# Optimization experiments

Hardware: AMD Instinct MI355X
Metric: run time of the kernel (lower is better)

## Reference

```python
import jax, jax.numpy as jnp
import numpy as np

HEADS = 8
DIM = 512
DIM_HEAD = 64          # dim // 8
LANDMARKS = 256        # dim // 2
PINV_ITERS = 6
KERNEL = 33            # residual depthwise conv kernel
EPS_LN = 1e-5


def setup_inputs() -> dict:
    key = jax.random.key(0)
    ks = jax.random.split(key, 4)
    b, n = 4, 4096
    x = jax.random.normal(ks[0], (b, n, DIM), dtype=jnp.float32)
    ln_g = jnp.ones((DIM,), jnp.float32)
    ln_b = jnp.zeros((DIM,), jnp.float32)
    w_qkv = jax.random.normal(ks[1], (3 * HEADS * DIM_HEAD, DIM), jnp.float32) * 0.02
    w_out = jax.random.normal(ks[2], (DIM, HEADS * DIM_HEAD), jnp.float32) * 0.02
    b_out = jnp.zeros((DIM,), jnp.float32)
    res_w = jax.random.normal(ks[3], (HEADS, 1, KERNEL, 1), jnp.float32) * 0.05
    return {"x": x, "ln_g": ln_g, "ln_b": ln_b, "w_qkv": w_qkv,
            "w_out": w_out, "b_out": b_out, "res_w": res_w}


def _moore_penrose_pinv(x, iters):
    # x: [b, h, m, m]; global (whole-tensor) max of row/col abs-sums, as in torch impl
    abs_x = jnp.abs(x)
    col = abs_x.sum(-1).max()
    row = abs_x.sum(-2).max()
    z = jnp.swapaxes(x, -1, -2) / (col * row)
    I = jnp.eye(x.shape[-1], dtype=x.dtype)
    for _ in range(iters):
        xz = x @ z
        z = 0.25 * z @ (13.0 * I - (xz @ (15.0 * I - (xz @ (7.0 * I - xz)))))
    return z


def reference(x, ln_g, ln_b, w_qkv, w_out, b_out, res_w):
    b, n, d = x.shape
    # pre-norm LayerNorm
    mu = x.mean(-1, keepdims=True)
    var = ((x - mu) ** 2).mean(-1, keepdims=True)
    xn = (x - mu) * jax.lax.rsqrt(var + EPS_LN) * ln_g + ln_b

    qkv = xn @ w_qkv.T                                  # [b, n, 3*h*dh]
    q, k, v = jnp.split(qkv, 3, axis=-1)
    to_heads = lambda t: t.reshape(b, n, HEADS, DIM_HEAD).transpose(0, 2, 1, 3)
    q = to_heads(q) * (DIM_HEAD ** -0.5)                # [b, h, n, dh]
    k = to_heads(k)
    v = to_heads(v)

    m = LANDMARKS
    l = n // m                                          # n chosen multiple of m (no pad)
    q_l = q.reshape(b, HEADS, m, l, DIM_HEAD).mean(3)   # [b, h, m, dh]
    k_l = k.reshape(b, HEADS, m, l, DIM_HEAD).mean(3)

    attn1 = jax.nn.softmax(jnp.einsum('bhid,bhjd->bhij', q, k_l), -1)    # [b,h,n,m]
    attn2 = jax.nn.softmax(jnp.einsum('bhid,bhjd->bhij', q_l, k_l), -1)  # [b,h,m,m]
    attn3 = jax.nn.softmax(jnp.einsum('bhid,bhjd->bhij', q_l, k), -1)    # [b,h,m,n]

    attn2_inv = _moore_penrose_pinv(attn2, PINV_ITERS)
    out = (attn1 @ attn2_inv) @ (attn3 @ v)             # [b, h, n, dh]

    # residual depthwise conv over sequence dim: v as NCHW (C=heads, H=n, W=dh)
    pad = KERNEL // 2
    res = jax.lax.conv_general_dilated(
        v, res_w, window_strides=(1, 1), padding=((pad, pad), (0, 0)),
        dimension_numbers=('NCHW', 'OIHW', 'NCHW'), feature_group_count=HEADS)
    out = out + res

    out = out.transpose(0, 2, 1, 3).reshape(b, n, HEADS * DIM_HEAD)
    out = out @ w_out.T + b_out                         # to_out Linear (dropout=eval identity)
    return x + out
```

## Files before the change

kernel.cpp:

```cpp
#include <hip/hip_runtime.h>
#include <hip/hip_bf16.h>
#include <math.h>


using bf16x8 = __attribute__((ext_vector_type(8))) short;
using f32x4  = __attribute__((ext_vector_type(4))) float;

static __device__ __forceinline__ f32x4 MFMA16(bf16x8 a, bf16x8 b, f32x4 c) {
    return __builtin_amdgcn_mfma_f32_16x16x32_bf16(a, b, c, 0, 0, 0);
}
static __device__ __forceinline__ unsigned short f2b(float f) {
    union { float f; unsigned u; } x; x.f = f;
    unsigned r = x.u + 0x7FFFu + ((x.u >> 16) & 1u);
    return (unsigned short)(r >> 16);
}
static __device__ __forceinline__ float b2f(unsigned short b) {
    union { unsigned u; float f; } x; x.u = ((unsigned)b) << 16; return x.f;
}

__global__ __launch_bounds__(256) void ln_kernel(const float* __restrict__ x,
                                                 const float* __restrict__ g,
                                                 const float* __restrict__ b,
                                                 unsigned short* __restrict__ xn) {
    int row = blockIdx.x;
    const float* xr = x + (size_t)row * 512;
    int t = threadIdx.x;
    float v0 = xr[t], v1 = xr[t + 256];
    __shared__ float red[4];
    float s = v0 + v1;
#pragma unroll
    for (int off = 32; off; off >>= 1) s += __shfl_down(s, off);
    if ((t & 63) == 0) red[t >> 6] = s;
    __syncthreads();
    float mean = (red[0] + red[1] + red[2] + red[3]) * (1.0f / 512.0f);
    __syncthreads();
    float d0 = v0 - mean, d1 = v1 - mean;
    float q2 = d0 * d0 + d1 * d1;
#pragma unroll
    for (int off = 32; off; off >>= 1) q2 += __shfl_down(q2, off);
    if ((t & 63) == 0) red[t >> 6] = q2;
    __syncthreads();
    float var = (red[0] + red[1] + red[2] + red[3]) * (1.0f / 512.0f);
    float inv = rsqrtf(var + 1e-5f);
    unsigned short* o = xn + (size_t)row * 512;
    o[t]       = f2b(d0 * inv * g[t]       + b[t]);
    o[t + 256] = f2b(d1 * inv * g[t + 256] + b[t + 256]);
}

__global__ void cvt_kernel(const float* __restrict__ wqkv, const float* __restrict__ wout,
                           unsigned short* __restrict__ wqkvb, unsigned short* __restrict__ woutb) {
    int idx = blockIdx.x * 256 + threadIdx.x;
    if (idx < 786432) wqkvb[idx] = f2b(wqkv[idx]);
    else woutb[idx - 786432] = f2b(wout[idx - 786432]);
}

template<int MODE>
__global__ __launch_bounds__(256) void gemm_mfma(const unsigned short* __restrict__ A,
                                                 const unsigned short* __restrict__ Bw,
                                                 unsigned short* __restrict__ qb,
                                                 unsigned short* __restrict__ kb,
                                                 unsigned short* __restrict__ vb,
                                                 const float* __restrict__ bias,
                                                 const float* __restrict__ xres,
                                                 float* __restrict__ out) {
    const int K = 512;
    __shared__ unsigned short As[128][40];
    __shared__ unsigned short Bs[128][40];
    int t = threadIdx.x;
    int w = t >> 6, l = t & 63, lr = l & 15, g = l >> 4;
    int wm = w >> 1, wn = w & 1;
    int row0 = blockIdx.x * 128, col0 = blockIdx.y * 128;
    f32x4 acc[4][4];
#pragma unroll
    for (int i = 0; i < 4; ++i)
#pragma unroll
        for (int j = 0; j < 4; ++j) acc[i][j] = (f32x4)0.f;
    int srow = t >> 1, sh = t & 1;
    for (int kt = 0; kt < K; kt += 32) {
        const unsigned short* as = A + (size_t)(row0 + srow) * K + kt + sh * 16;
        *(uint4*)&As[srow][sh * 16]     = *(const uint4*)as;
        *(uint4*)&As[srow][sh * 16 + 8] = *(const uint4*)(as + 8);
        const unsigned short* bs = Bw + (size_t)(col0 + srow) * K + kt + sh * 16;
        *(uint4*)&Bs[srow][sh * 16]     = *(const uint4*)bs;
        *(uint4*)&Bs[srow][sh * 16 + 8] = *(const uint4*)(bs + 8);
        __syncthreads();
        bf16x8 a[4], b[4];
#pragma unroll
        for (int mt = 0; mt < 4; ++mt) a[mt] = *(const bf16x8*)&As[wm * 64 + mt * 16 + lr][g * 8];
#pragma unroll
        for (int nt = 0; nt < 4; ++nt) b[nt] = *(const bf16x8*)&Bs[wn * 64 + nt * 16 + lr][g * 8];
#pragma unroll
        for (int mt = 0; mt < 4; ++mt)
#pragma unroll
            for (int nt = 0; nt < 4; ++nt) acc[mt][nt] = MFMA16(a[mt], b[nt], acc[mt][nt]);
        __syncthreads();
    }
#pragma unroll
    for (int mt = 0; mt < 4; ++mt) {
#pragma unroll
        for (int nt = 0; nt < 4; ++nt) {
#pragma unroll
            for (int r = 0; r < 4; ++r) {
                int row = row0 + wm * 64 + mt * 16 + g * 4 + r;
                int col = col0 + wn * 64 + nt * 16 + lr;
                float val = acc[mt][nt][r];
                if (MODE == 0) {
                    int bb = row >> 12, nn = row & 4095;
                    int which = col >> 9, rem = col & 511;
                    int hh = rem >> 6, dd = rem & 63;
                    size_t di = (((size_t)(bb * 8 + hh)) * 4096 + nn) * 64 + dd;
                    if (which == 0) qb[di] = f2b(val * 0.125f);
                    else if (which == 1) kb[di] = f2b(val);
                    else vb[di] = f2b(val);
                } else {
                    out[(size_t)row * 512 + col] = val + bias[col] + xres[(size_t)row * 512 + col];
                }
            }
        }
    }
}

__global__ __launch_bounds__(256) void vt_kernel(const unsigned short* __restrict__ vb,
                                                 unsigned short* __restrict__ vtb) {
    int n0 = blockIdx.x * 64, bh = blockIdx.y;
    __shared__ unsigned short tl[64][72];
    int t = threadIdx.x;
#pragma unroll
    for (int u = 0; u < 2; ++u) {
        int cid = t * 2 + u;
        int r = cid >> 3, c8 = (cid & 7) << 3;
        uint4 vv = *(const uint4*)(vb + ((size_t)bh * 4096 + n0 + r) * 64 + c8);
        unsigned short* pv = (unsigned short*)&vv;
#pragma unroll
        for (int i = 0; i < 8; ++i) tl[c8 + i][r] = pv[i];
    }
    __syncthreads();
#pragma unroll
    for (int u = 0; u < 2; ++u) {
        int cid = t * 2 + u;
        int r = cid >> 3, c8 = (cid & 7) << 3;
        *(uint4*)(vtb + ((size_t)bh * 64 + r) * 4096 + n0 + c8) = *(uint4*)&tl[r][c8];
    }
}

__global__ void landmark_kernel(const unsigned short* __restrict__ q,
                                const unsigned short* __restrict__ k,
                                float* __restrict__ ql, float* __restrict__ kl,
                                unsigned short* __restrict__ qlb, unsigned short* __restrict__ klb,
                                unsigned short* __restrict__ qll, unsigned short* __restrict__ kll) {
    int idx = blockIdx.x * 256 + threadIdx.x;
    int dh = idx & 63, mi = (idx >> 6) & 255, bh = idx >> 14;
    size_t base = ((size_t)bh * 4096 + mi * 16) * 64 + dh;
    float sq = 0, sk = 0;
#pragma unroll
    for (int j = 0; j < 16; ++j) { sq += b2f(q[base + (size_t)j * 64]); sk += b2f(k[base + (size_t)j * 64]); }
    sq *= 0.0625f; sk *= 0.0625f;
    ql[idx] = sq; kl[idx] = sk;
    unsigned short qh = f2b(sq), kh = f2b(sk);
    qlb[idx] = qh; klb[idx] = kh;
    qll[idx] = f2b(sq - b2f(qh));
    kll[idx] = f2b(sk - b2f(kh));
}

__global__ __launch_bounds__(256) void conv_kernel(const unsigned short* __restrict__ v,
                                                   const float* __restrict__ rw,
                                                   float* __restrict__ outh) {
    int idx = blockIdx.x * 256 + threadIdx.x;
    int o = idx & 7, n = (idx >> 3) & 4095, bh = idx >> 15;
    int h = bh & 7;
    const unsigned short* vb = v + (((size_t)bh) << 18) + o * 8;
    float acc[8];
#pragma unroll
    for (int i = 0; i < 8; ++i) acc[i] = 0.f;
#pragma unroll
    for (int tt = 0; tt < 33; ++tt) {
        int j = n + tt - 16;
        if (j >= 0 && j < 4096) {
            uint4 pv = *(const uint4*)(vb + (size_t)j * 64);
            const unsigned short* pp = (const unsigned short*)&pv;
            float wgt = rw[h * 33 + tt];
#pragma unroll
            for (int i = 0; i < 8; ++i) acc[i] = fmaf(wgt, b2f(pp[i]), acc[i]);
        }
    }
    float4 r0, r1;
    r0.x = acc[0]; r0.y = acc[1]; r0.z = acc[2]; r0.w = acc[3];
    r1.x = acc[4]; r1.y = acc[5]; r1.z = acc[6]; r1.w = acc[7];
    *(float4*)(outh + (size_t)idx * 8)     = r0;
    *(float4*)(outh + (size_t)idx * 8 + 4) = r1;
}

__global__ __launch_bounds__(256) void attn2_mfma(const unsigned short* __restrict__ qlh,
                                                  const unsigned short* __restrict__ qllo,
                                                  const unsigned short* __restrict__ klh,
                                                  const unsigned short* __restrict__ kllo,
                                                  float* __restrict__ a2) {
    int it = blockIdx.x, bh = blockIdx.y;
    __shared__ unsigned short qh_l[64][72], ql_l[64][72];
    __shared__ unsigned short kh_l[128][72], kl_l[128][72];
    int t = threadIdx.x;
    int w = t >> 6, l = t & 63, lr = l & 15, g = l >> 4;
    int i0 = it * 64;
    int srow = t >> 2, sq = t & 3;
    {
        size_t gi = ((size_t)bh * 256 + i0 + srow) * 64 + sq * 16;
        *(uint4*)&qh_l[srow][sq * 16]     = *(const uint4*)(qlh + gi);
        *(uint4*)&qh_l[srow][sq * 16 + 8] = *(const uint4*)(qlh + gi + 8);
        *(uint4*)&ql_l[srow][sq * 16]     = *(const uint4*)(qllo + gi);
        *(uint4*)&ql_l[srow][sq * 16 + 8] = *(const uint4*)(qllo + gi + 8);
    }
    f32x4 p[16];
    float tsum[4] = {0.f, 0.f, 0.f, 0.f};
    bf16x8 ah0, ah1, al0, al1;
#pragma unroll
    for (int ph = 0; ph < 2; ++ph) {
        __syncthreads();
#pragma unroll
        for (int st = 0; st < 2; ++st) {
            int row = st * 64 + srow;
            size_t gi = ((size_t)bh * 256 + ph * 128 + row) * 64 + sq * 16;
            *(uint4*)&kh_l[row][sq * 16]     = *(const uint4*)(klh + gi);
            *(uint4*)&kh_l[row][sq * 16 + 8] = *(const uint4*)(klh + gi + 8);
            *(uint4*)&kl_l[row][sq * 16]     = *(const uint4*)(kllo + gi);
            *(uint4*)&kl_l[row][sq * 16 + 8] = *(const uint4*)(kllo + gi + 8);
        }
        __syncthreads();
        if (ph == 0) {
            ah0 = *(const bf16x8*)&qh_l[w * 16 + lr][g * 8];
            ah1 = *(const bf16x8*)&qh_l[w * 16 + lr][32 + g * 8];
            al0 = *(const bf16x8*)&ql_l[w * 16 + lr][g * 8];
            al1 = *(const bf16x8*)&ql_l[w * 16 + lr][32 + g * 8];
        }
#pragma unroll
        for (int f = 0; f < 8; ++f) {
            bf16x8 bh0 = *(const bf16x8*)&kh_l[f * 16 + lr][g * 8];
            bf16x8 bh1 = *(const bf16x8*)&kh_l[f * 16 + lr][32 + g * 8];
            bf16x8 bl0 = *(const bf16x8*)&kl_l[f * 16 + lr][g * 8];
            bf16x8 bl1 = *(const bf16x8*)&kl_l[f * 16 + lr][32 + g * 8];
            f32x4 s = (f32x4)0.f;
            s = MFMA16(ah0, bh0, s); s = MFMA16(ah1, bh1, s);
            s = MFMA16(ah0, bl0, s); s = MFMA16(ah1, bl1, s);
            s = MFMA16(al0, bh0, s); s = MFMA16(al1, bh1, s);
            f32x4 pe;
#pragma unroll
            for (int r = 0; r < 4; ++r) { pe[r] = __expf(s[r]); tsum[r] += pe[r]; }
            p[ph * 8 + f] = pe;
        }
    }
#pragma unroll
    for (int r = 0; r < 4; ++r) {
#pragma unroll
        for (int m = 1; m < 16; m <<= 1) tsum[r] += __shfl_xor(tsum[r], m);
    }
#pragma unroll
    for (int f = 0; f < 16; ++f) {
#pragma unroll
        for (int r = 0; r < 4; ++r) {
            a2[((size_t)bh * 256 + i0 + w * 16 + g * 4 + r) * 256 + f * 16 + lr] = p[f][r] / tsum[r];
        }
    }
}

__global__ __launch_bounds__(256) void colmax_kernel(const float* __restrict__ a2,
                                                     unsigned* __restrict__ scal) {
    int bh = blockIdx.x, t = threadIdx.x;
    const float* m = a2 + (size_t)bh * 65536;
    float cs = 0;
    for (int i = 0; i < 256; ++i) cs += m[i * 256 + t];
#pragma unroll
    for (int off = 32; off; off >>= 1) cs = fmaxf(cs, __shfl_down(cs, off));
    __shared__ float red[4];
    if ((t & 63) == 0) red[t >> 6] = cs;
    __syncthreads();
    if (t == 0) {
        float mx = fmaxf(fmaxf(red[0], red[1]), fmaxf(red[2], red[3]));
        atomicMax(scal, __float_as_uint(mx));
    }
}

__global__ __launch_bounds__(256) void z0_split(const float* __restrict__ a2,
                                                const float* __restrict__ scal,
                                                float* __restrict__ zf,
                                                unsigned short* __restrict__ zh,
                                                unsigned short* __restrict__ zl) {
    int bh = blockIdx.z;
    int ib = blockIdx.x * 64, jb = blockIdx.y * 64;
    __shared__ float tl[64][65];
    float c = 1.0f / *scal;
    int t = threadIdx.x;
#pragma unroll
    for (int u = 0; u < 16; ++u) {
        int idx = t + 256 * u;
        int r = idx >> 6, cc = idx & 63;
        tl[r][cc] = a2[(size_t)bh * 65536 + (size_t)(jb + r) * 256 + ib + cc];
    }
    __syncthreads();
#pragma unroll
    for (int u = 0; u < 16; ++u) {
        int idx = t + 256 * u;
        int r = idx >> 6, cc = idx & 63;
        float v = tl[cc][r] * c;
        unsigned short hi = f2b(v);
        size_t di = (size_t)bh * 65536 + (size_t)(ib + r) * 256 + jb + cc;
        zf[di] = v;
        zh[di] = hi;
        zl[di] = f2b(v - b2f(hi));
    }
}

__global__ void split_kernel(const float* __restrict__ src,
                             unsigned short* __restrict__ dh,
                             unsigned short* __restrict__ dl) {
    int idx4 = (blockIdx.x * 256 + threadIdx.x) * 4;
    float4 v = *(const float4*)(src + idx4);
    float vv[4] = {v.x, v.y, v.z, v.w};
    ushort4 h4, l4;
    unsigned short* hp = (unsigned short*)&h4;
    unsigned short* lp = (unsigned short*)&l4;
#pragma unroll
    for (int j = 0; j < 4; ++j) {
        unsigned short hi = f2b(vv[j]);
        hp[j] = hi;
        lp[j] = f2b(vv[j] - b2f(hi));
    }
    *(ushort4*)(dh + idx4) = h4;
    *(ushort4*)(dl + idx4) = l4;
}

__global__ __launch_bounds__(256) void bgemm_split2(const unsigned short* __restrict__ Ahg,
                                                    const unsigned short* __restrict__ Alg,
                                                    const unsigned short* __restrict__ Bhg,
                                                    const unsigned short* __restrict__ Blg,
                                                    unsigned short* __restrict__ Dh,
                                                    unsigned short* __restrict__ Dl,
                                                    float* __restrict__ Df,
                                                    const float* __restrict__ Ef,
                                                    float alpha, float gamma) {
    size_t so = (size_t)blockIdx.z * 65536;
    Ahg += so; Alg += so; Bhg += so; Blg += so; Dh += so; Dl += so; Df += so;
    const float* Efp = Ef ? Ef + so : nullptr;
    __shared__ unsigned short Ah[64][40], Al[64][40], Bh2[64][40], Bl2[64][40];
    int t = threadIdx.x;
    int w = t >> 6, l = t & 63, lr = l & 15, g = l >> 4;
    int wm = w >> 1, wn = w & 1;
    int bm = blockIdx.x, bn = blockIdx.y;
    f32x4 acc[2][2];
#pragma unroll
    for (int i = 0; i < 2; ++i)
#pragma unroll
        for (int j = 0; j < 2; ++j) acc[i][j] = (f32x4)0.f;
    int arow = t >> 2, akq = (t & 3) * 8;
    int bkr = t >> 3, bnq = (t & 7) * 8;
    for (int kt = 0; kt < 256; kt += 32) {
        size_t ai = (size_t)(bm * 64 + arow) * 256 + kt + akq;
        *(uint4*)&Ah[arow][akq] = *(const uint4*)(Ahg + ai);
        *(uint4*)&Al[arow][akq] = *(const uint4*)(Alg + ai);
        size_t bi = (size_t)(kt + bkr) * 256 + bn * 64 + bnq;
        uint4 bhv = *(const uint4*)(Bhg + bi);
        uint4 blv = *(const uint4*)(Blg + bi);
        const unsigned short* bhp = (const unsigned short*)&bhv;
        const unsigned short* blp = (const unsigned short*)&blv;
#pragma unroll
        for (int i = 0; i < 8; ++i) {
            Bh2[bnq + i][bkr] = bhp[i];
            Bl2[bnq + i][bkr] = blp[i];
        }
        __syncthreads();
        bf16x8 ah[2], al_[2], bh[2], bl_[2];
#pragma unroll
        for (int mf = 0; mf < 2; ++mf) {
            ah[mf]  = *(const bf16x8*)&Ah[wm * 32 + mf * 16 + lr][g * 8];
            al_[mf] = *(const bf16x8*)&Al[wm * 32 + mf * 16 + lr][g * 8];
        }
#pragma unroll
        for (int nf = 0; nf < 2; ++nf) {
            bh[nf]  = *(const bf16x8*)&Bh2[wn * 32 + nf * 16 + lr][g * 8];
            bl_[nf] = *(const bf16x8*)&Bl2[wn * 32 + nf * 16 + lr][g * 8];
        }
#pragma unroll
        for (int mf = 0; mf < 2; ++mf)
#pragma unroll
            for (int nf = 0; nf < 2; ++nf) {
                acc[mf][nf] = MFMA16(ah[mf], bh[nf], acc[mf][nf]);
                acc[mf][nf] = MFMA16(ah[mf], bl_[nf], acc[mf][nf]);
                acc[mf][nf] = MFMA16(al_[mf], bh[nf], acc[mf][nf]);
            }
        __syncthreads();
    }
#pragma unroll
    for (int mf = 0; mf < 2; ++mf) {
#pragma unroll
        for (int nf = 0; nf < 2; ++nf) {
#pragma unroll
            for (int r = 0; r < 4; ++r) {
                int row = bm * 64 + wm * 32 + mf * 16 + g * 4 + r;
                int col = bn * 64 + wn * 32 + nf * 16 + lr;
                size_t di = (size_t)row * 256 + col;
                float val = alpha * acc[mf][nf][r];
                if (Efp) val = fmaf(gamma, Efp[di], val);
                Df[di] = val;
                unsigned short hi = f2b(val);
                Dh[di] = hi;
                Dl[di] = f2b(val - b2f(hi));
            }
        }
    }
}

__global__ __launch_bounds__(256) void bgemm_w2t(const float* __restrict__ A,
                                                 const float* __restrict__ B,
                                                 unsigned short* __restrict__ w2t) {
    const int M = 256, N = 64, K = 256;
    int s = blockIdx.z;
    int bm = blockIdx.x;
    A += (size_t)s * M * K; B += (size_t)s * K * N;
    __shared__ float As[32][67];
    __shared__ float Bs[32][68];
    int t = threadIdx.x;
    int tm = t & 15, tn = t >> 4;
    float acc[4][4];
#pragma unroll
    for (int i = 0; i < 4; ++i)
#pragma unroll
        for (int j = 0; j < 4; ++j) acc[i][j] = 0.f;
    for (int kt = 0; kt < K; kt += 32) {
#pragma unroll
        for (int u = 0; u < 2; ++u) {
            int fid = t + 256 * u;
            int r = fid >> 3, kg = (fid & 7) << 2;
            float4 av = *(const float4*)(A + (size_t)(bm * 64 + r) * K + kt + kg);
            As[kg + 0][r] = av.x; As[kg + 1][r] = av.y; As[kg + 2][r] = av.z; As[kg + 3][r] = av.w;
            int kr = fid >> 4, cg = (fid & 15) << 2;
            if (cg < N) {
                float4 bv = *(const float4*)(B + (size_t)(kt + kr) * N + cg);
                *(float4*)(&Bs[kr][cg]) = bv;
            }
        }
        __syncthreads();
#pragma unroll
        for (int kk = 0; kk < 32; ++kk) {
            float a[4], bb[4];
#pragma unroll
            for (int i = 0; i < 4; ++i) a[i] = As[kk][tm * 4 + i];
#pragma unroll
            for (int j = 0; j < 4; ++j) bb[j] = Bs[kk][(tn & 15) * 4 + j];
#pragma unroll
            for (int i = 0; i < 4; ++i)
#pragma unroll
                for (int j = 0; j < 4; ++j) acc[i][j] = fmaf(a[i], bb[j], acc[i][j]);
        }
        __syncthreads();
    }
    if (tn < 16) {
#pragma unroll
        for (int i = 0; i < 4; ++i) {
            int r = bm * 64 + tm * 4 + i;
#pragma unroll
            for (int j = 0; j < 4; ++j) {
                int c = tn * 4 + j;
                w2t[(size_t)s * 16384 + (size_t)c * 256 + r] = f2b(acc[i][j]);
            }
        }
    }
}

__global__ __launch_bounds__(256) void attn3v_mfma(const unsigned short* __restrict__ qlb,
                                                   const unsigned short* __restrict__ kb,
                                                   const unsigned short* __restrict__ vtb,
                                                   float* __restrict__ num_part,
                                                   float* __restrict__ den_part) {
    int it = blockIdx.x, js = blockIdx.y, bh = blockIdx.z;
    __shared__ unsigned short k_lds[64][72];
    __shared__ unsigned short v_lds[64][72];
    __shared__ unsigned short p_lds[4][16][72];
    int t = threadIdx.x;
    int w = t >> 6, l = t & 63, lr = l & 15, g = l >> 4;
    int i0 = it * 64;
    const unsigned short* qp = qlb + ((size_t)(bh * 256 + i0 + w * 16 + lr)) * 64 + g * 8;
    bf16x8 aq0 = *(const bf16x8*)qp;
    bf16x8 aq1 = *(const bf16x8*)(qp + 32);
    f32x4 acc[4];
#pragma unroll
    for (int i = 0; i < 4; ++i) acc[i] = (f32x4)0.f;
    float dacc[4] = {0.f, 0.f, 0.f, 0.f};
    int srow = t >> 2, sq = t & 3;
    const size_t kbase = ((size_t)bh * 4096 + js * 1024) * 64;
    const size_t vbase = (size_t)bh * 64 * 4096 + js * 1024;
    for (int st = 0; st < 16; ++st) {
        int j0 = st * 64;
        {
            const unsigned short* src = kb + kbase + (size_t)(j0 + srow) * 64 + sq * 16;
            *(uint4*)&k_lds[srow][sq * 16]     = *(const uint4*)src;
            *(uint4*)&k_lds[srow][sq * 16 + 8] = *(const uint4*)(src + 8);
            const unsigned short* sv = vtb + vbase + (size_t)srow * 4096 + j0 + sq * 16;
            *(uint4*)&v_lds[srow][sq * 16]     = *(const uint4*)sv;
            *(uint4*)&v_lds[srow][sq * 16 + 8] = *(const uint4*)(sv + 8);
        }
        __syncthreads();
        f32x4 sacc[4];
#pragma unroll
        for (int jt = 0; jt < 4; ++jt) {
            bf16x8 bk0 = *(const bf16x8*)&k_lds[jt * 16 + lr][g * 8];
            bf16x8 bk1 = *(const bf16x8*)&k_lds[jt * 16 + lr][32 + g * 8];
            sacc[jt] = MFMA16(aq0, bk0, (f32x4)0.f);
            sacc[jt] = MFMA16(aq1, bk1, sacc[jt]);
        }
        float dr[4] = {0.f, 0.f, 0.f, 0.f};
#pragma unroll
        for (int jt = 0; jt < 4; ++jt) {
#pragma unroll
            for (int r = 0; r < 4; ++r) {
                float p = __expf(sacc[jt][r]);
                p_lds[w][g * 4 + r][jt * 16 + lr] = f2b(p);
                dr[r] += p;
            }
        }
#pragma unroll
        for (int r = 0; r < 4; ++r) {
#pragma unroll
            for (int m = 1; m < 16; m <<= 1) dr[r] += __shfl_xor(dr[r], m);
            dacc[r] += dr[r];
        }
        bf16x8 pa0 = *(const bf16x8*)&p_lds[w][lr][g * 8];
        bf16x8 pa1 = *(const bf16x8*)&p_lds[w][lr][32 + g * 8];
#pragma unroll
        for (int dt = 0; dt < 4; ++dt) {
            bf16x8 bv0 = *(const bf16x8*)&v_lds[dt * 16 + lr][g * 8];
            bf16x8 bv1 = *(const bf16x8*)&v_lds[dt * 16 + lr][32 + g * 8];
            acc[dt] = MFMA16(pa0, bv0, acc[dt]);
            acc[dt] = MFMA16(pa1, bv1, acc[dt]);
        }
        __syncthreads();
    }
    size_t obase = (size_t)(js * 32 + bh) * 256 + i0 + w * 16;
#pragma unroll
    for (int dt = 0; dt < 4; ++dt)
#pragma unroll
        for (int r = 0; r < 4; ++r)
            num_part[(obase + g * 4 + r) * 64 + dt * 16 + lr] = acc[dt][r];
    if (lr == 0) {
#pragma unroll
        for (int r = 0; r < 4; ++r) den_part[obase + g * 4 + r] = dacc[r];
    }
}

__global__ void a3v_combine(const float* __restrict__ num_part,
                            const float* __restrict__ den_part,
                            float* __restrict__ a3v) {
    int idx = blockIdx.x * 256 + threadIdx.x;
    int dh = idx & 63;
    int rest = idx >> 6;
    float n = 0, d = 0;
#pragma unroll
    for (int s = 0; s < 4; ++s) {
        n += num_part[((size_t)s * 8192 + rest) * 64 + dh];
        d += den_part[(size_t)s * 8192 + rest];
    }
    a3v[idx] = n / d;
}

__global__ __launch_bounds__(256) void attn1_mfma(const unsigned short* __restrict__ qb,
                                                  const unsigned short* __restrict__ klb,
                                                  const unsigned short* __restrict__ w2t,
                                                  const float* __restrict__ outh,
                                                  unsigned short* __restrict__ outhb) {
    int it = blockIdx.x, bh = blockIdx.y;
    __shared__ unsigned short k_lds[64][72];
    __shared__ unsigned short v_lds[64][72];
    __shared__ unsigned short p_lds[4][16][72];
    int t = threadIdx.x;
    int w = t >> 6, l = t & 63, lr = l & 15, g = l >> 4;
    int i0 = it * 64;
    const unsigned short* qp = qb + ((size_t)bh * 4096 + i0 + w * 16 + lr) * 64 + g * 8;
    bf16x8 aq0 = *(const bf16x8*)qp;
    bf16x8 aq1 = *(const bf16x8*)(qp + 32);
    f32x4 acc[4];
#pragma unroll
    for (int i = 0; i < 4; ++i) acc[i] = (f32x4)0.f;
    float dacc[4] = {0.f, 0.f, 0.f, 0.f};
    int srow = t >> 2, sq = t & 3;
    for (int st = 0; st < 4; ++st) {
        int j0 = st * 64;
        {
            const unsigned short* src = klb + ((size_t)bh * 256 + j0 + srow) * 64 + sq * 16;
            *(uint4*)&k_lds[srow][sq * 16]     = *(const uint4*)src;
            *(uint4*)&k_lds[srow][sq * 16 + 8] = *(const uint4*)(src + 8);
            const unsigned short* sv = w2t + ((size_t)bh * 64 + srow) * 256 + j0 + sq * 16;
            *(uint4*)&v_lds[srow][sq * 16]     = *(const uint4*)sv;
            *(uint4*)&v_lds[srow][sq * 16 + 8] = *(const uint4*)(sv + 8);
        }
        __syncthreads();
        f32x4 sacc[4];
#pragma unroll
        for (int jt = 0; jt < 4; ++jt) {
            bf16x8 bk0 = *(const bf16x8*)&k_lds[jt * 16 + lr][g * 8];
            bf16x8 bk1 = *(const bf16x8*)&k_lds[jt * 16 + lr][32 + g * 8];
            sacc[jt] = MFMA16(aq0, bk0, (f32x4)0.f);
            sacc[jt] = MFMA16(aq1, bk1, sacc[jt]);
        }
        float dr[4] = {0.f, 0.f, 0.f, 0.f};
#pragma unroll
        for (int jt = 0; jt < 4; ++jt) {
#pragma unroll
            for (int r = 0; r < 4; ++r) {
                float p = __expf(sacc[jt][r]);
                p_lds[w][g * 4 + r][jt * 16 + lr] = f2b(p);
                dr[r] += p;
            }
        }
#pragma unroll
        for (int r = 0; r < 4; ++r) {
#pragma unroll
            for (int m = 1; m < 16; m <<= 1) dr[r] += __shfl_xor(dr[r], m);
            dacc[r] += dr[r];
        }
        bf16x8 pa0 = *(const bf16x8*)&p_lds[w][lr][g * 8];
        bf16x8 pa1 = *(const bf16x8*)&p_lds[w][lr][32 + g * 8];
#pragma unroll
        for (int dt = 0; dt < 4; ++dt) {
            bf16x8 bv0 = *(const bf16x8*)&v_lds[dt * 16 + lr][g * 8];
            bf16x8 bv1 = *(const bf16x8*)&v_lds[dt * 16 + lr][32 + g * 8];
            acc[dt] = MFMA16(pa0, bv0, acc[dt]);
            acc[dt] = MFMA16(pa1, bv1, acc[dt]);
        }
        __syncthreads();
    }
    int bb = bh >> 3, hh = bh & 7;
#pragma unroll
    for (int dt = 0; dt < 4; ++dt) {
#pragma unroll
        for (int r = 0; r < 4; ++r) {
            int row = i0 + w * 16 + g * 4 + r;
            float val = acc[dt][r] / dacc[r]
                      + outh[((size_t)bh * 4096 + row) * 64 + dt * 16 + lr];
            outhb[((size_t)(bb * 4096 + row)) * 512 + hh * 64 + dt * 16 + lr] = f2b(val);
        }
    }
}

extern "C" void kernel_launch(void* const* d_in, const int* in_sizes, int n_in,
                              void* d_out, int out_size, void* d_ws, size_t ws_size,
                              hipStream_t stream) {
    (void)in_sizes; (void)n_in; (void)out_size; (void)ws_size;
    const float* x     = (const float*)d_in[0];
    const float* ln_g  = (const float*)d_in[1];
    const float* ln_b  = (const float*)d_in[2];
    const float* w_qkv = (const float*)d_in[3];
    const float* w_out = (const float*)d_in[4];
    const float* b_out = (const float*)d_in[5];
    const float* res_w = (const float*)d_in[6];
    float* out = (float*)d_out;

    float* ws = (float*)d_ws;
    unsigned short* xnb = (unsigned short*)ws;
    float* num_part = ws;
    float* den_part = ws + 2097152;
    float* a3v      = ws + 2129920;
    unsigned short* outhb = (unsigned short*)ws;
    float* outh = ws + 4194304;
    float* ql   = ws + 12582912;
    float* kl   = ws + 13107200;
    float* a2   = ws + 13631488;
    float* z0f  = ws + 15728640;
    float* z1f  = ws + 17825792;
    float* xzf  = ws + 19922944;
    unsigned* scal = (unsigned*)(ws + 22020096);
    unsigned short* a2h = (unsigned short*)(ws + 22020100);
    unsigned short* a2l = (unsigned short*)(ws + 23068676);
    unsigned short* z0h = (unsigned short*)(ws + 24117252);
    unsigned short* z0l = (unsigned short*)(ws + 25165828);
    unsigned short* z1h = (unsigned short*)(ws + 26214404);
    unsigned short* z1l = (unsigned short*)(ws + 27262980);
    unsigned short* xzh = (unsigned short*)(ws + 28311556);
    unsigned short* xzl = (unsigned short*)(ws + 29360132);
    unsigned short* t1h = (unsigned short*)(ws + 30408708);
    unsigned short* t1l = (unsigned short*)(ws + 31457284);
    unsigned short* t2h = (unsigned short*)(ws + 32505860);
    unsigned short* t2l = (unsigned short*)(ws + 33554436);
    unsigned short* qb  = (unsigned short*)(ws + 34603012);
    unsigned short* kb  = (unsigned short*)(ws + 38797316);
    unsigned short* vb  = (unsigned short*)(ws + 42991620);
    unsigned short* vtb = (unsigned short*)(ws + 47185924);
    unsigned short* qlb   = (unsigned short*)(ws + 51380228);
    unsigned short* klb   = (unsigned short*)(ws + 51642372);
    unsigned short* qll   = (unsigned short*)(ws + 51904516);
    unsigned short* kll   = (unsigned short*)(ws + 52166660);
    unsigned short* wqkvb = (unsigned short*)(ws + 52428804);
    unsigned short* woutb = (unsigned short*)(ws + 52822020);
    unsigned short* w2tb  = (unsigned short*)(ws + 52953092);

    hipMemsetAsync(scal, 0, 4, stream);
    ln_kernel<<<16384, 256, 0, stream>>>(x, ln_g, ln_b, xnb);
    cvt_kernel<<<4096, 256, 0, stream>>>(w_qkv, w_out, wqkvb, woutb);
    gemm_mfma<0><<<dim3(128, 12), 256, 0, stream>>>(xnb, wqkvb, qb, kb, vb, nullptr, nullptr, nullptr);
    vt_kernel<<<dim3(64, 32), 256, 0, stream>>>(vb, vtb);
    landmark_kernel<<<2048, 256, 0, stream>>>(qb, kb, ql, kl, qlb, klb, qll, kll);
    conv_kernel<<<4096, 256, 0, stream>>>(vb, res_w, outh);
    attn2_mfma<<<dim3(4, 32), 256, 0, stream>>>(qlb, qll, klb, kll, a2);
    colmax_kernel<<<32, 256, 0, stream>>>(a2, scal);
    z0_split<<<dim3(4, 4, 32), 256, 0, stream>>>(a2, (const float*)scal, z0f, z0h, z0l);
    split_kernel<<<2048, 256, 0, stream>>>(a2, a2h, a2l);
    unsigned short *zch = z0h, *zcl = z0l, *zah = z1h, *zal = z1l;
    float *zcf = z0f, *zaf = z1f;
    float* dfscratch = a2;
    for (int itr = 0; itr < 6; ++itr) {
        bgemm_split2<<<dim3(4, 4, 32), 256, 0, stream>>>(a2h, a2l, zch, zcl, xzh, xzl, xzf, nullptr, 1.f, 0.f);
        bgemm_split2<<<dim3(4, 4, 32), 256, 0, stream>>>(xzh, xzl, xzh, xzl, t1h, t1l, dfscratch, xzf, -1.f, 7.f);
        bgemm_split2<<<dim3(4, 4, 32), 256, 0, stream>>>(xzh, xzl, t1h, t1l, t2h, t2l, dfscratch, xzf, -1.f, 15.f);
        bgemm_split2<<<dim3(4, 4, 32), 256, 0, stream>>>(zch, zcl, t2h, t2l, zah, zal, zaf, zcf, -0.25f, 3.25f);
        unsigned short* th = zch; zch = zah; zah = th;
        unsigned short* tl2 = zcl; zcl = zal; zal = tl2;
        float* tf = zcf; zcf = zaf; zaf = tf;
    }
    attn3v_mfma<<<dim3(4, 4, 32), 256, 0, stream>>>(qlb, kb, vtb, num_part, den_part);
    a3v_combine<<<2048, 256, 0, stream>>>(num_part, den_part, a3v);
    bgemm_w2t<<<dim3(4, 1, 32), 256, 0, stream>>>(zcf, a3v, w2tb);
    attn1_mfma<<<dim3(64, 32), 256, 0, stream>>>(qb, klb, w2tb, outh, outhb);
    gemm_mfma<1><<<dim3(128, 4), 256, 0, stream>>>(outhb, woutb, nullptr, nullptr, nullptr, b_out, x, out);
}
```

Measured before the change: 868.5 us.

## Use direct global-to-LDS loads and transposed split operands in pinv GEMMs

Replaces the register-staged LDS fills in the main GEMM and the pinv batched GEMMs with global_load_lds direct copies into XOR-swizzled LDS tiles. The pinv GEMMs now write transposed hi/lo bf16 copies of their outputs, so the B operand is read in natural row-major K order. This removes the scalar transpose scatter into LDS and the fp32 side buffers. The final z·a3v product moves from an fp32 FMA kernel onto the MFMA split-bf16 GEMM. The trade is extra transposed stores, plus small accuracy changes from rebuilding the epilogue E term out of hi+lo bf16 instead of fp32.

```diff
diff --git a/kernel.cpp b/kernel.cpp
--- a/kernel.cpp
+++ b/kernel.cpp
@@ -16,6 +16,11 @@
 }
 static __device__ __forceinline__ float b2f(unsigned short b) {
     union { unsigned u; float f; } x; x.u = ((unsigned)b) << 16; return x.f;
+}
+static __device__ __forceinline__ void gload16(const unsigned short* g, void* l) {
+    __builtin_amdgcn_global_load_lds(
+        (const __attribute__((address_space(1))) unsigned int*)g,
+        (__attribute__((address_space(3))) unsigned int*)l, 16, 0, 0);
 }
 
 __global__ __launch_bounds__(256) void ln_kernel(const float* __restrict__ x,
@@ -63,32 +68,35 @@
                                                  const float* __restrict__ bias,
                                                  const float* __restrict__ xres,
                                                  float* __restrict__ out) {
-    const int K = 512;
-    __shared__ unsigned short As[128][40];
-    __shared__ unsigned short Bs[128][40];
+    __shared__ unsigned char LA[8192];
+    __shared__ unsigned char LB[8192];
     int t = threadIdx.x;
     int w = t >> 6, l = t & 63, lr = l & 15, g = l >> 4;
     int wm = w >> 1, wn = w & 1;
+    int il = l >> 2;
+    int gsrc = (l & 3) ^ ((l >> 3) & 3);
     int row0 = blockIdx.x * 128, col0 = blockIdx.y * 128;
     f32x4 acc[4][4];
 #pragma unroll
     for (int i = 0; i < 4; ++i)
 #pragma unroll
         for (int j = 0; j < 4; ++j) acc[i][j] = (f32x4)0.f;
-    int srow = t >> 1, sh = t & 1;
-    for (int kt = 0; kt < K; kt += 32) {
-        const unsigned short* as = A + (size_t)(row0 + srow) * K + kt + sh * 16;
-        *(uint4*)&As[srow][sh * 16]     = *(const uint4*)as;
-        *(uint4*)&As[srow][sh * 16 + 8] = *(const uint4*)(as + 8);
-        const unsigned short* bs = Bw + (size_t)(col0 + srow) * K + kt + sh * 16;
-        *(uint4*)&Bs[srow][sh * 16]     = *(const uint4*)bs;
-        *(uint4*)&Bs[srow][sh * 16 + 8] = *(const uint4*)(bs + 8);
+    int so = ((lr >> 1) & 3) ^ g;
+    for (int kt = 0; kt < 512; kt += 32) {
+#pragma unroll
+        for (int j = 0; j < 2; ++j) {
+            int c = w + 4 * j;
+            gload16(A  + (size_t)(row0 + c * 16 + il) * 512 + kt + gsrc * 8, &LA[c * 1024]);
+            gload16(Bw + (size_t)(col0 + c * 16 + il) * 512 + kt + gsrc * 8, &LB[c * 1024]);
+        }
         __syncthreads();
         bf16x8 a[4], b[4];
 #pragma unroll
-        for (int mt = 0; mt < 4; ++mt) a[mt] = *(const bf16x8*)&As[wm * 64 + mt * 16 + lr][g * 8];
-#pragma unroll
-        for (int nt = 0; nt < 4; ++nt) b[nt] = *(const bf16x8*)&Bs[wn * 64 + nt * 16 + lr][g * 8];
+        for (int mt = 0; mt < 4; ++mt)
+            a[mt] = *(const bf16x8*)&LA[(wm * 64 + mt * 16 + lr) * 64 + so * 16];
+#pragma unroll
+        for (int nt = 0; nt < 4; ++nt)
+            b[nt] = *(const bf16x8*)&LB[(wn * 64 + nt * 16 + lr) * 64 + so * 16];
 #pragma unroll
         for (int mt = 0; mt < 4; ++mt)
 #pragma unroll
@@ -278,11 +286,32 @@
     }
 }
 
-__global__ __launch_bounds__(256) void z0_split(const float* __restrict__ a2,
-                                                const float* __restrict__ scal,
-                                                float* __restrict__ zf,
-                                                unsigned short* __restrict__ zh,
-                                                unsigned short* __restrict__ zl) {
+__global__ void split_scale_kernel(const float* __restrict__ src, const float* __restrict__ scal,
+                                   unsigned short* __restrict__ a2h, unsigned short* __restrict__ a2l,
+                                   unsigned short* __restrict__ zth, unsigned short* __restrict__ ztl) {
+    float c = 1.0f / *scal;
+    int idx4 = (blockIdx.x * 256 + threadIdx.x) * 4;
+    float4 v = *(const float4*)(src + idx4);
+    float vv[4] = {v.x, v.y, v.z, v.w};
+    ushort4 h4, l4, sh4, sl4;
+    unsigned short* hp = (unsigned short*)&h4;  unsigned short* lp = (unsigned short*)&l4;
+    unsigned short* shp = (unsigned short*)&sh4; unsigned short* slp = (unsigned short*)&sl4;
+#pragma unroll
+    for (int j = 0; j < 4; ++j) {
+        unsigned short hi = f2b(vv[j]);
+        hp[j] = hi; lp[j] = f2b(vv[j] - b2f(hi));
+        float sv = vv[j] * c;
+        unsigned short shi = f2b(sv);
+        shp[j] = shi; slp[j] = f2b(sv - b2f(shi));
+    }
+    *(ushort4*)(a2h + idx4) = h4;  *(ushort4*)(a2l + idx4) = l4;
+    *(ushort4*)(zth + idx4) = sh4; *(ushort4*)(ztl + idx4) = sl4;
+}
+
+__global__ __launch_bounds__(256) void z0pair_kernel(const float* __restrict__ a2,
+                                                     const float* __restrict__ scal,
+                                                     unsigned short* __restrict__ zh,
+                                                     unsigned short* __restrict__ zl) {
     int bh = blockIdx.z;
     int ib = blockIdx.x * 64, jb = blockIdx.y * 64;
     __shared__ float tl[64][65];
@@ -302,163 +331,111 @@
         float v = tl[cc][r] * c;
         unsigned short hi = f2b(v);
         size_t di = (size_t)bh * 65536 + (size_t)(ib + r) * 256 + jb + cc;
-        zf[di] = v;
         zh[di] = hi;
         zl[di] = f2b(v - b2f(hi));
     }
 }
 
-__global__ void split_kernel(const float* __restrict__ src,
-                             unsigned short* __restrict__ dh,
-                             unsigned short* __restrict__ dl) {
-    int idx4 = (blockIdx.x * 256 + threadIdx.x) * 4;
-    float4 v = *(const float4*)(src + idx4);
-    float vv[4] = {v.x, v.y, v.z, v.w};
-    ushort4 h4, l4;
-    unsigned short* hp = (unsigned short*)&h4;
-    unsigned short* lp = (unsigned short*)&l4;
-#pragma unroll
-    for (int j = 0; j < 4; ++j) {
-        unsigned short hi = f2b(vv[j]);
-        hp[j] = hi;
-        lp[j] = f2b(vv[j] - b2f(hi));
-    }
-    *(ushort4*)(dh + idx4) = h4;
-    *(ushort4*)(dl + idx4) = l4;
-}
-
-__global__ __launch_bounds__(256) void bgemm_split2(const unsigned short* __restrict__ Ahg,
-                                                    const unsigned short* __restrict__ Alg,
-                                                    const unsigned short* __restrict__ Bhg,
-                                                    const unsigned short* __restrict__ Blg,
-                                                    unsigned short* __restrict__ Dh,
-                                                    unsigned short* __restrict__ Dl,
-                                                    float* __restrict__ Df,
-                                                    const float* __restrict__ Ef,
-                                                    float alpha, float gamma) {
-    size_t so = (size_t)blockIdx.z * 65536;
-    Ahg += so; Alg += so; Bhg += so; Blg += so; Dh += so; Dl += so; Df += so;
-    const float* Efp = Ef ? Ef + so : nullptr;
-    __shared__ unsigned short Ah[64][40], Al[64][40], Bh2[64][40], Bl2[64][40];
+template<int WD, int WDT, int SGL>
+__global__ __launch_bounds__(256) void bgemm_nat(
+        const unsigned short* __restrict__ Xh, const unsigned short* __restrict__ Xl,
+        const unsigned short* __restrict__ Yh, const unsigned short* __restrict__ Yl,
+        unsigned short* __restrict__ Dh, unsigned short* __restrict__ Dl,
+        unsigned short* __restrict__ DTh, unsigned short* __restrict__ DTl,
+        const unsigned short* __restrict__ Eh, const unsigned short* __restrict__ El,
+        float alpha, float gamma,
+        unsigned int sX, unsigned int sY, unsigned int sD, unsigned int sDT) {
+    int s = blockIdx.z;
+    const unsigned short* Xhp = Xh + (size_t)s * sX;
+    const unsigned short* Xlp = Xl + (size_t)s * sX;
+    const unsigned short* Yhp = Yh + (size_t)s * sY;
+    const unsigned short* Ylp = Yl + (size_t)s * sY;
+    const unsigned short* Ehp = Eh ? Eh + (size_t)s * 65536 : nullptr;
+    const unsigned short* Elp = El ? El + (size_t)s * 65536 : nullptr;
+    __shared__ unsigned char LXh[4096], LXl[4096], LYh[4096], LYl[4096];
     int t = threadIdx.x;
     int w = t >> 6, l = t & 63, lr = l & 15, g = l >> 4;
     int wm = w >> 1, wn = w & 1;
+    int il = l >> 2;
+    int gsrc = (l & 3) ^ ((l >> 3) & 3);
     int bm = blockIdx.x, bn = blockIdx.y;
     f32x4 acc[2][2];
 #pragma unroll
     for (int i = 0; i < 2; ++i)
 #pragma unroll
         for (int j = 0; j < 2; ++j) acc[i][j] = (f32x4)0.f;
-    int arow = t >> 2, akq = (t & 3) * 8;
-    int bkr = t >> 3, bnq = (t & 7) * 8;
+    int so = ((lr >> 1) & 3) ^ g;
+    size_t xro = (size_t)(bm * 64 + w * 16 + il) * 256;
+    size_t yro = (size_t)(bn * 64 + w * 16 + il) * 256;
     for (int kt = 0; kt < 256; kt += 32) {
-        size_t ai = (size_t)(bm * 64 + arow) * 256 + kt + akq;
-        *(uint4*)&Ah[arow][akq] = *(const uint4*)(Ahg + ai);
-        *(uint4*)&Al[arow][akq] = *(const uint4*)(Alg + ai);
-        size_t bi = (size_t)(kt + bkr) * 256 + bn * 64 + bnq;
-        uint4 bhv = *(const uint4*)(Bhg + bi);
-        uint4 blv = *(const uint4*)(Blg + bi);
-        const unsigned short* bhp = (const unsigned short*)&bhv;
-        const unsigned short* blp = (const unsigned short*)&blv;
-#pragma unroll
-        for (int i = 0; i < 8; ++i) {
-            Bh2[bnq + i][bkr] = bhp[i];
-            Bl2[bnq + i][bkr] = blp[i];
-        }
-        __syncthreads();
-        bf16x8 ah[2], al_[2], bh[2], bl_[2];
+        gload16(Xhp + xro + kt + gsrc * 8, &LXh[w * 1024]);
+        gload16(Xlp + xro + kt + gsrc * 8, &LXl[w * 1024]);
+        gload16(Yhp + yro + kt + gsrc * 8, &LYh[w * 1024]);
+        gload16(Ylp + yro + kt + gsrc * 8, &LYl[w * 1024]);
+        __syncthreads();
+        bf16x8 xh[2], xl_[2], yh[2], yl_[2];
 #pragma unroll
         for (int mf = 0; mf < 2; ++mf) {
-            ah[mf]  = *(const bf16x8*)&Ah[wm * 32 + mf * 16 + lr][g * 8];
-            al_[mf] = *(const bf16x8*)&Al[wm * 32 + mf * 16 + lr][g * 8];
+            int off = (wm * 32 + mf * 16 + lr) * 64 + so * 16;
+            xh[mf]  = *(const bf16x8*)&LXh[off];
+            xl_[mf] = *(const bf16x8*)&LXl[off];
         }
 #pragma unroll
         for (int nf = 0; nf < 2; ++nf) {
-            bh[nf]  = *(const bf16x8*)&Bh2[wn * 32 + nf * 16 + lr][g * 8];
-            bl_[nf] = *(const bf16x8*)&Bl2[wn * 32 + nf * 16 + lr][g * 8];
+            int off = (wn * 32 + nf * 16 + lr) * 64 + so * 16;
+            yh[nf]  = *(const bf16x8*)&LYh[off];
+            yl_[nf] = *(const bf16x8*)&LYl[off];
         }
 #pragma unroll
         for (int mf = 0; mf < 2; ++mf)
 #pragma unroll
             for (int nf = 0; nf < 2; ++nf) {
-                acc[mf][nf] = MFMA16(ah[mf], bh[nf], acc[mf][nf]);
-                acc[mf][nf] = MFMA16(ah[mf], bl_[nf], acc[mf][nf]);
-                acc[mf][nf] = MFMA16(al_[mf], bh[nf], acc[mf][nf]);
+                acc[mf][nf] = MFMA16(xh[mf], yh[nf], acc[mf][nf]);
+                acc[mf][nf] = MFMA16(xh[mf], yl_[nf], acc[mf][nf]);
+                acc[mf][nf] = MFMA16(xl_[mf], yh[nf], acc[mf][nf]);
             }
         __syncthreads();
     }
+    size_t dbase = (size_t)s * sD;
+    size_t tbase = (size_t)s * sDT;
 #pragma unroll
     for (int mf = 0; mf < 2; ++mf) {
 #pragma unroll
         for (int nf = 0; nf < 2; ++nf) {
+            int rb = bm * 64 + wm * 32 + mf * 16 + g * 4;
+            int col = bn * 64 + wn * 32 + nf * 16 + lr;
+            float v4[4];
 #pragma unroll
             for (int r = 0; r < 4; ++r) {
-                int row = bm * 64 + wm * 32 + mf * 16 + g * 4 + r;
-                int col = bn * 64 + wn * 32 + nf * 16 + lr;
-                size_t di = (size_t)row * 256 + col;
                 float val = alpha * acc[mf][nf][r];
-                if (Efp) val = fmaf(gamma, Efp[di], val);
-                Df[di] = val;
-                unsigned short hi = f2b(val);
-                Dh[di] = hi;
-                Dl[di] = f2b(val - b2f(hi));
+                if (Ehp) {
+                    size_t ei = (size_t)(rb + r) * 256 + col;
+                    val = fmaf(gamma, b2f(Ehp[ei]) + b2f(Elp[ei]), val);
+                }
+                v4[r] = val;
             }
-        }
-    }
-}
-
-__global__ __launch_bounds__(256) void bgemm_w2t(const float* __restrict__ A,
-                                                 const float* __restrict__ B,
-                                                 unsigned short* __restrict__ w2t) {
-    const int M = 256, N = 64, K = 256;
-    int s = blockIdx.z;
-    int bm = blockIdx.x;
-    A += (size_t)s * M * K; B += (size_t)s * K * N;
-    __shared__ float As[32][67];
-    __shared__ float Bs[32][68];
-    int t = threadIdx.x;
-    int tm = t & 15, tn = t >> 4;
-    float acc[4][4];
-#pragma unroll
-    for (int i = 0; i < 4; ++i)
-#pragma unroll
-        for (int j = 0; j < 4; ++j) acc[i][j] = 0.f;
-    for (int kt = 0; kt < K; kt += 32) {
-#pragma unroll
-        for (int u = 0; u < 2; ++u) {
-            int fid = t + 256 * u;
-            int r = fid >> 3, kg = (fid & 7) << 2;
-            float4 av = *(const float4*)(A + (size_t)(bm * 64 + r) * K + kt + kg);
-            As[kg + 0][r] = av.x; As[kg + 1][r] = av.y; As[kg + 2][r] = av.z; As[kg + 3][r] = av.w;
-            int kr = fid >> 4, cg = (fid & 15) << 2;
-            if (cg < N) {
-                float4 bv = *(const float4*)(B + (size_t)(kt + kr) * N + cg);
-                *(float4*)(&Bs[kr][cg]) = bv;
+            if (WD) {
+#pragma unroll
+                for (int r = 0; r < 4; ++r) {
+                    size_t di = dbase + (size_t)(rb + r) * 256 + col;
+                    unsigned short hi = f2b(v4[r]);
+                    Dh[di] = hi;
+                    if (!SGL) Dl[di] = f2b(v4[r] - b2f(hi));
+                }
             }
-        }
-        __syncthreads();
-#pragma unroll
-        for (int kk = 0; kk < 32; ++kk) {
-            float a[4], bb[4];
-#pragma unroll
-            for (int i = 0; i < 4; ++i) a[i] = As[kk][tm * 4 + i];
-#pragma unroll
-            for (int j = 0; j < 4; ++j) bb[j] = Bs[kk][(tn & 15) * 4 + j];
-#pragma unroll
-            for (int i = 0; i < 4; ++i)
-#pragma unroll
-                for (int j = 0; j < 4; ++j) acc[i][j] = fmaf(a[i], bb[j], acc[i][j]);
-        }
-        __syncthreads();
-    }
-    if (tn < 16) {
-#pragma unroll
-        for (int i = 0; i < 4; ++i) {
-            int r = bm * 64 + tm * 4 + i;
-#pragma unroll
-            for (int j = 0; j < 4; ++j) {
-                int c = tn * 4 + j;
-                w2t[(size_t)s * 16384 + (size_t)c * 256 + r] = f2b(acc[i][j]);
+            if (WDT) {
+                ushort4 hh, ll;
+                unsigned short* hp = (unsigned short*)&hh;
+                unsigned short* lp = (unsigned short*)&ll;
+#pragma unroll
+                for (int r = 0; r < 4; ++r) {
+                    unsigned short hi = f2b(v4[r]);
+                    hp[r] = hi;
+                    lp[r] = f2b(v4[r] - b2f(hi));
+                }
+                size_t ti = tbase + (size_t)col * 256 + rb;
+                *(ushort4*)(DTh + ti) = hh;
+                *(ushort4*)(DTl + ti) = ll;
             }
         }
     }
@@ -546,17 +523,21 @@
 
 __global__ void a3v_combine(const float* __restrict__ num_part,
                             const float* __restrict__ den_part,
-                            float* __restrict__ a3v) {
+                            unsigned short* __restrict__ th,
+                            unsigned short* __restrict__ tlo) {
     int idx = blockIdx.x * 256 + threadIdx.x;
-    int dh = idx & 63;
-    int rest = idx >> 6;
+    int i = idx & 255, dh = (idx >> 8) & 63, bh = idx >> 14;
+    int rest = bh * 256 + i;
     float n = 0, d = 0;
 #pragma unroll
     for (int s = 0; s < 4; ++s) {
         n += num_part[((size_t)s * 8192 + rest) * 64 + dh];
         d += den_part[(size_t)s * 8192 + rest];
     }
-    a3v[idx] = n / d;
+    float v = n / d;
+    unsigned short hi = f2b(v);
+    th[idx] = hi;
+    tlo[idx] = f2b(v - b2f(hi));
 }
 
 __global__ __launch_bounds__(256) void attn1_mfma(const unsigned short* __restrict__ qb,
@@ -655,40 +636,45 @@
     unsigned short* xnb = (unsigned short*)ws;
     float* num_part = ws;
     float* den_part = ws + 2097152;
-    float* a3v      = ws + 2129920;
+    unsigned short* a3vTh = (unsigned short*)(ws + 2129920);
+    unsigned short* a3vTl = (unsigned short*)(ws + 2392064);
     unsigned short* outhb = (unsigned short*)ws;
     float* outh = ws + 4194304;
     float* ql   = ws + 12582912;
     float* kl   = ws + 13107200;
-    float* a2   = ws + 13631488;
-    float* z0f  = ws + 15728640;
-    float* z1f  = ws + 17825792;
-    float* xzf  = ws + 19922944;
-    unsigned* scal = (unsigned*)(ws + 22020096);
-    unsigned short* a2h = (unsigned short*)(ws + 22020100);
-    unsigned short* a2l = (unsigned short*)(ws + 23068676);
-    unsigned short* z0h = (unsigned short*)(ws + 24117252);
-    unsigned short* z0l = (unsigned short*)(ws + 25165828);
-    unsigned short* z1h = (unsigned short*)(ws + 26214404);
-    unsigned short* z1l = (unsigned short*)(ws + 27262980);
-    unsigned short* xzh = (unsigned short*)(ws + 28311556);
-    unsigned short* xzl = (unsigned short*)(ws + 29360132);
-    unsigned short* t1h = (unsigned short*)(ws + 30408708);
-    unsigned short* t1l = (unsigned short*)(ws + 31457284);
-    unsigned short* t2h = (unsigned short*)(ws + 32505860);
-    unsigned short* t2l = (unsigned short*)(ws + 33554436);
-    unsigned short* qb  = (unsigned short*)(ws + 34603012);
-    unsigned short* kb  = (unsigned short*)(ws + 38797316);
-    unsigned short* vb  = (unsigned short*)(ws + 42991620);
-    unsigned short* vtb = (unsigned short*)(ws + 47185924);
-    unsigned short* qlb   = (unsigned short*)(ws + 51380228);
-    unsigned short* klb   = (unsigned short*)(ws + 51642372);
-    unsigned short* qll   = (unsigned short*)(ws + 51904516);
-    unsigned short* kll   = (unsigned short*)(ws + 52166660);
-    unsigned short* wqkvb = (unsigned short*)(ws + 52428804);
-    unsigned short* woutb = (unsigned short*)(ws + 52822020);
-    unsigned short* w2tb  = (unsigned short*)(ws + 52953092);
-
+    float* a2f  = ws + 13631488;
+    unsigned* scal = (unsigned*)(ws + 15728640);
+    unsigned short* a2h  = (unsigned short*)(ws + 15728648);
+    unsigned short* a2l  = (unsigned short*)(ws + 16777224);
+    unsigned short* zAh  = (unsigned short*)(ws + 17825800);
+    unsigned short* zAl  = (unsigned short*)(ws + 18874376);
+    unsigned short* zAth = (unsigned short*)(ws + 19922952);
+    unsigned short* zAtl = (unsigned short*)(ws + 20971528);
+    unsigned short* zBh  = (unsigned short*)(ws + 22020104);
+    unsigned short* zBl  = (unsigned short*)(ws + 23068680);
+    unsigned short* zBth = (unsigned short*)(ws + 24117256);
+    unsigned short* zBtl = (unsigned short*)(ws + 25165832);
+    unsigned short* xzh  = (unsigned short*)(ws + 26214408);
+    unsigned short* xzl  = (unsigned short*)(ws + 27262984);
+    unsigned short* xzth = (unsigned short*)(ws + 28311560);
+    unsigned short* xztl = (unsigned short*)(ws + 29360136);
+    unsigned short* t1th = (unsigned short*)(ws + 30408712);
+    unsigned short* t1tl = (unsigned short*)(ws + 31457288);
+    unsigned short* t2th = (unsigned short*)(ws + 32505864);
+    unsigned short* t2tl = (unsigned short*)(ws + 33554440);
+    unsigned short* qb  = (unsigned short*)(ws + 34603016);
+    unsigned short* kb  = (unsigned short*)(ws + 38797320);
+    unsigned short* vb  = (unsigned short*)(ws + 42991624);
+    unsigned short* vtb = (unsigned short*)(ws + 47185928);
+    unsigned short* qlb = (unsigned short*)(ws + 51380232);
+    unsigned short* klb = (unsigned short*)(ws + 51642376);
+    unsigned short* qll = (unsigned short*)(ws + 51904520);
+    unsigned short* kll = (unsigned short*)(ws + 52166664);
+    unsigned short* wqkvb = (unsigned short*)(ws + 52428808);
+    unsigned short* woutb = (unsigned short*)(ws + 52822024);
+    unsigned short* w2tb  = (unsigned short*)(ws + 52953096);
+
+    const unsigned int S = 65536u;
     hipMemsetAsync(scal, 0, 4, stream);
     ln_kernel<<<16384, 256, 0, stream>>>(x, ln_g, ln_b, xnb);
     cvt_kernel<<<4096, 256, 0, stream>>>(w_qkv, w_out, wqkvb, woutb);
@@ -696,25 +682,30 @@
     vt_kernel<<<dim3(64, 32), 256, 0, stream>>>(vb, vtb);
     landmark_kernel<<<2048, 256, 0, stream>>>(qb, kb, ql, kl, qlb, klb, qll, kll);
     conv_kernel<<<4096, 256, 0, stream>>>(vb, res_w, outh);
-    attn2_mfma<<<dim3(4, 32), 256, 0, stream>>>(qlb, qll, klb, kll, a2);
-    colmax_kernel<<<32, 256, 0, stream>>>(a2, scal);
-    z0_split<<<dim3(4, 4, 32), 256, 0, stream>>>(a2, (const float*)scal, z0f, z0h, z0l);
-    split_kernel<<<2048, 256, 0, stream>>>(a2, a2h, a2l);
-    unsigned short *zch = z0h, *zcl = z0l, *zah = z1h, *zal = z1l;
-    float *zcf = z0f, *zaf = z1f;
-    float* dfscratch = a2;
+    attn2_mfma<<<dim3(4, 32), 256, 0, stream>>>(qlb, qll, klb, kll, a2f);
+    colmax_kernel<<<32, 256, 0, stream>>>(a2f, scal);
+    split_scale_kernel<<<2048, 256, 0, stream>>>(a2f, (const float*)scal, a2h, a2l, zAth, zAtl);
+    z0pair_kernel<<<dim3(4, 4, 32), 256, 0, stream>>>(a2f, (const float*)scal, zAh, zAl);
+    unsigned short *zh = zAh, *zl = zAl, *zth = zAth, *ztl = zAtl;
+    unsigned short *nh = zBh, *nl = zBl, *nth = zBth, *ntl = zBtl;
     for (int itr = 0; itr < 6; ++itr) {
-        bgemm_split2<<<dim3(4, 4, 32), 256, 0, stream>>>(a2h, a2l, zch, zcl, xzh, xzl, xzf, nullptr, 1.f, 0.f);
-        bgemm_split2<<<dim3(4, 4, 32), 256, 0, stream>>>(xzh, xzl, xzh, xzl, t1h, t1l, dfscratch, xzf, -1.f, 7.f);
-        bgemm_split2<<<dim3(4, 4, 32), 256, 0, stream>>>(xzh, xzl, t1h, t1l, t2h, t2l, dfscratch, xzf, -1.f, 15.f);
-        bgemm_split2<<<dim3(4, 4, 32), 256, 0, stream>>>(zch, zcl, t2h, t2l, zah, zal, zaf, zcf, -0.25f, 3.25f);
-        unsigned short* th = zch; zch = zah; zah = th;
-        unsigned short* tl2 = zcl; zcl = zal; zal = tl2;
-        float* tf = zcf; zcf = zaf; zaf = tf;
+        bgemm_nat<1, 1, 0><<<dim3(4, 4, 32), 256, 0, stream>>>(
+            a2h, a2l, zth, ztl, xzh, xzl, xzth, xztl, nullptr, nullptr, 1.f, 0.f, S, S, S, S);
+        bgemm_nat<0, 1, 0><<<dim3(4, 4, 32), 256, 0, stream>>>(
+            xzh, xzl, xzth, xztl, nullptr, nullptr, t1th, t1tl, xzh, xzl, -1.f, 7.f, S, S, S, S);
+        bgemm_nat<0, 1, 0><<<dim3(4, 4, 32), 256, 0, stream>>>(
+            xzh, xzl, t1th, t1tl, nullptr, nullptr, t2th, t2tl, xzh, xzl, -1.f, 15.f, S, S, S, S);
+        bgemm_nat<1, 1, 0><<<dim3(4, 4, 32), 256, 0, stream>>>(
+            zh, zl, t2th, t2tl, nh, nl, nth, ntl, zh, zl, -0.25f, 3.25f, S, S, S, S);
+        unsigned short* tp;
+        tp = zh; zh = nh; nh = tp;   tp = zl; zl = nl; nl = tp;
+        tp = zth; zth = nth; nth = tp; tp = ztl; ztl = ntl; ntl = tp;
     }
     attn3v_mfma<<<dim3(4, 4, 32), 256, 0, stream>>>(qlb, kb, vtb, num_part, den_part);
-    a3v_combine<<<2048, 256, 0, stream>>>(num_part, den_part, a3v);
-    bgemm_w2t<<<dim3(4, 1, 32), 256, 0, stream>>>(zcf, a3v, w2tb);
+    a3v_combine<<<2048, 256, 0, stream>>>(num_part, den_part, a3vTh, a3vTl);
+    bgemm_nat<1, 0, 1><<<dim3(1, 4, 32), 256, 0, stream>>>(
+        a3vTh, a3vTl, zh, zl, w2tb, nullptr, nullptr, nullptr, nullptr, nullptr,
+        1.f, 0.f, 16384u, S, 16384u, S);
     attn1_mfma<<<dim3(64, 32), 256, 0, stream>>>(qb, klb, w2tb, outh, outhb);
     gemm_mfma<1><<<dim3(128, 4), 256, 0, stream>>>(outhb, woutb, nullptr, nullptr, nullptr, b_out, x, out);
 }
```

Result: faster. 780.6 us (-10.1%).
